# Kernel tuning notes

Measured on AMD Instinct MI355X. Metric: run time of the kernel, lower is better.

## Reference

```python
import jax, jax.numpy as jnp
import numpy as np
from jax import lax

SCORE_THRESH = 0.05
NMS_THRESH = 0.5
DETECTIONS_PER_IMG = 100
MIN_SIZE = 0.01
AREA_THRESH = 0.0
BOX_W = (10.0, 10.0, 5.0, 5.0)
BBOX_XFORM_CLIP = float(np.log(1000.0 / 16.0))


def setup_inputs() -> dict:
    key = jax.random.key(0)
    B, N, C = 8, 4000, 91
    H, W = 800, 1333
    k1, k2, k3 = jax.random.split(key, 3)
    # scale logits so a realistic fraction of softmax scores exceed score_thresh
    class_logits = jax.random.normal(k1, (B * N, C), jnp.float32) * 2.0
    box_regression = jax.random.normal(k2, (B * N, C * 4), jnp.float32)
    u = jax.random.uniform(k3, (B, N, 4), jnp.float32)
    x1 = u[..., 0] * (W - 50)
    y1 = u[..., 1] * (H - 50)
    bw = u[..., 2] * 200.0 + 4.0
    bh = u[..., 3] * 200.0 + 4.0
    proposals = jnp.stack([x1, y1, jnp.minimum(x1 + bw, W), jnp.minimum(y1 + bh, H)], axis=-1)
    return {"class_logits": class_logits, "box_regression": box_regression,
            "proposals": proposals, "image_h": H, "image_w": W}


def _decode(rel, props):
    # torchvision BoxCoder.decode: props [P,4], rel [P, C*4] -> [P, C, 4]
    w = props[:, 2] - props[:, 0]
    h = props[:, 3] - props[:, 1]
    cx = props[:, 0] + 0.5 * w
    cy = props[:, 1] + 0.5 * h
    rel = rel.reshape(rel.shape[0], -1, 4)
    dx = rel[..., 0] / BOX_W[0]
    dy = rel[..., 1] / BOX_W[1]
    dw = jnp.minimum(rel[..., 2] / BOX_W[2], BBOX_XFORM_CLIP)
    dh = jnp.minimum(rel[..., 3] / BOX_W[3], BBOX_XFORM_CLIP)
    pcx = dx * w[:, None] + cx[:, None]
    pcy = dy * h[:, None] + cy[:, None]
    pw = jnp.exp(dw) * w[:, None]
    ph = jnp.exp(dh) * h[:, None]
    return jnp.stack([pcx - 0.5 * pw, pcy - 0.5 * ph, pcx + 0.5 * pw, pcy + 0.5 * ph], axis=-1)


def _nms_image(boxes, scores, labels_f, valid, off_unit):
    # greedy batched NMS (class-offset trick) producing first DETECTIONS_PER_IMG survivors
    NEG = -1e9
    s0 = jnp.where(valid, scores, NEG)
    ob = boxes + (labels_f * off_unit)[:, None]  # per-class coordinate offset
    areas = (ob[:, 2] - ob[:, 0]) * (ob[:, 3] - ob[:, 1])

    def step(s, _):
        i = jnp.argmax(s)
        sc = s[i]
        ok = sc > (NEG / 2)
        obi = ob[i]
        ix1 = jnp.maximum(obi[0], ob[:, 0])
        iy1 = jnp.maximum(obi[1], ob[:, 1])
        ix2 = jnp.minimum(obi[2], ob[:, 2])
        iy2 = jnp.minimum(obi[3], ob[:, 3])
        inter = jnp.maximum(ix2 - ix1, 0.0) * jnp.maximum(iy2 - iy1, 0.0)
        ai = (obi[2] - obi[0]) * (obi[3] - obi[1])
        iou = inter / jnp.maximum(ai + areas - inter, 1e-9)
        sup = (iou > NMS_THRESH) & ok
        s = jnp.where(sup, NEG, s).at[i].set(NEG)
        return s, (i, jnp.where(ok, sc, 0.0), ok)

    _, (idx, out_sc, ok) = lax.scan(step, s0, None, length=DETECTIONS_PER_IMG)
    out_boxes = boxes[idx] * ok[:, None]
    out_labels = jnp.where(ok, labels_f[idx], 0.0)
    areas_out = (out_boxes[:, 2] - out_boxes[:, 0]) * (out_boxes[:, 3] - out_boxes[:, 1])
    keep = ok & (areas_out >= AREA_THRESH)
    return out_boxes * keep[:, None], out_sc * keep, jnp.where(keep, out_labels, 0.0), keep


def reference(class_logits, box_regression, proposals, image_h, image_w):
    B, N, _ = proposals.shape
    C = class_logits.shape[-1]
    pred_boxes = _decode(box_regression, proposals.reshape(B * N, 4)).reshape(B, N, C, 4)
    pred_scores = jax.nn.softmax(class_logits, axis=-1).reshape(B, N, C)
    # clip boxes to image
    x = jnp.clip(pred_boxes[..., 0::2], 0.0, float(image_w))
    y = jnp.clip(pred_boxes[..., 1::2], 0.0, float(image_h))
    pred_boxes = jnp.stack([x[..., 0], y[..., 0], x[..., 1], y[..., 1]], axis=-1)
    # drop background class 0, flatten (proposal, class) pairs
    M = N * (C - 1)
    boxes = pred_boxes[:, :, 1:, :].reshape(B, M, 4)
    scores = pred_scores[:, :, 1:].reshape(B, M)
    labels_f = jnp.broadcast_to(jnp.arange(1, C, dtype=boxes.dtype)[None, :], (N, C - 1)).reshape(M)
    ws = boxes[..., 2] - boxes[..., 0]
    hs = boxes[..., 3] - boxes[..., 1]
    valid = (scores > SCORE_THRESH) & (ws >= MIN_SIZE) & (hs >= MIN_SIZE)
    off_unit = float(max(image_h, image_w)) + 1.0
    out_boxes, out_scores, out_labels_f, keep = jax.vmap(
        lambda b, s, v: _nms_image(b, s, labels_f, v, off_unit))(boxes, scores, valid)
    return out_boxes, out_scores, out_labels_f.astype(jnp.int32), keep
```

## Files before the change

kernel.cpp:

```cpp
#include <hip/hip_runtime.h>
#include <stdint.h>

typedef uint32_t u32;
typedef unsigned long long u64;

#define NB 8
#define NPER 4000
#define NC 91
#define NCLS 90
#define NDET 100
#define CHUNKS 64
#define RPB 63
#define LBIN 16
#define CCAP 63
#define BINCAP 512
#define SURVCAP 9216
#define NSFIX (NCLS * NDET)
#define FKCAP 1024
#define VPT 36

__device__ __forceinline__ float4 decode_clip(float4 rel, float w, float h,
                                              float cx, float cy, float W, float H) {
  const float XCLIP = 4.135166556742356f;
  float dx = rel.x / 10.0f;
  float dy = rel.y / 10.0f;
  float dw = fminf(rel.z / 5.0f, XCLIP);
  float dh = fminf(rel.w / 5.0f, XCLIP);
  float qcx = dx * w + cx;
  float qcy = dy * h + cy;
  float qw = expf(dw) * w;
  float qh = expf(dh) * h;
  float x1 = qcx - 0.5f * qw, y1 = qcy - 0.5f * qh;
  float x2 = qcx + 0.5f * qw, y2 = qcy + 0.5f * qh;
  x1 = fminf(fmaxf(x1, 0.0f), W);
  x2 = fminf(fmaxf(x2, 0.0f), W);
  y1 = fminf(fmaxf(y1, 0.0f), H);
  y2 = fminf(fmaxf(y2, 0.0f), H);
  return make_float4(x1, y1, x2, y2);
}

__device__ __forceinline__ float rdlane(float v, int sl) {
  return __int_as_float(__builtin_amdgcn_readlane(__float_as_int(v), sl));
}

__global__ __launch_bounds__(1024) void k_score(const float* __restrict__ logits,
    const float* __restrict__ boxreg, const float* __restrict__ props,
    const int* __restrict__ dh, const int* __restrict__ dw,
    u32* cnt_g, u64* bins_key, float4* bins_box) {
  __shared__ u64 s_key[NCLS][LBIN];
  __shared__ float4 s_box[NCLS][LBIN];
  __shared__ u32 s_cnt[NCLS];
  int tid = threadIdx.x;
  int b = blockIdx.x / CHUNKS;
  int chunk = blockIdx.x % CHUNKS;
  int wave = tid >> 6, lane = tid & 63;
  if (tid < NCLS) s_cnt[tid] = 0u;
  __syncthreads();

  float H = (float)dh[0], W = (float)dw[0];
  const float4* props4 = (const float4*)props;
  const float4* breg4 = (const float4*)boxreg;
  size_t chbase = ((size_t)(b * CHUNKS + chunk)) * NCLS;

  for (int rloc = wave; rloc < RPB; rloc += 16) {
    int rl = chunk * RPB + rloc;
    if (rl >= NPER) break;
    int r = b * NPER + rl;
    const float* lrow = logits + (size_t)r * NC;
    float xA = lrow[lane];
    float xB = (lane < NC - 64) ? lrow[64 + lane] : -3.0e38f;
    float mx = fmaxf(xA, xB);
    for (int o = 32; o; o >>= 1) mx = fmaxf(mx, __shfl_xor(mx, o));
    float eA = expf(xA - mx);
    float eB = (lane < NC - 64) ? expf(xB - mx) : 0.0f;
    float sm = eA + eB;
    for (int o = 32; o; o >>= 1) sm += __shfl_xor(sm, o);
    float sA = eA / sm;
    float sB = eB / sm;
    bool eA_ok = (lane >= 1) && (sA > 0.05f);
    bool eB_ok = (lane < NC - 64) && (sB > 0.05f);
    if (eA_ok || eB_ok) {
      float4 p = props4[r];
      float w = p.z - p.x, h = p.w - p.y;
      float cx = p.x + 0.5f * w, cy = p.y + 0.5f * h;
      if (eA_ok) {
        float4 raw = decode_clip(breg4[(size_t)r * NC + lane], w, h, cx, cy, W, H);
        if (((raw.z - raw.x) >= 0.01f) && ((raw.w - raw.y) >= 0.01f)) {
          int ci = lane - 1;
          u32 orig = (u32)(rl * NCLS + ci);
          u64 key = ((u64)__float_as_uint(sA) << 22) | (u64)(0x3FFFFFu - orig);
          u32 lp = atomicAdd(&s_cnt[ci], 1u);
          if (lp < LBIN) { s_key[ci][lp] = key; s_box[ci][lp] = raw; }
          else if (lp < CCAP) {
            size_t o = (chbase + ci) * CCAP + lp;
            bins_key[o] = key; bins_box[o] = raw;
          }
        }
      }
      if (eB_ok) {
        float4 raw = decode_clip(breg4[(size_t)r * NC + 64 + lane], w, h, cx, cy, W, H);
        if (((raw.z - raw.x) >= 0.01f) && ((raw.w - raw.y) >= 0.01f)) {
          int ci = 63 + lane;
          u32 orig = (u32)(rl * NCLS + ci);
          u64 key = ((u64)__float_as_uint(sB) << 22) | (u64)(0x3FFFFFu - orig);
          u32 lp = atomicAdd(&s_cnt[ci], 1u);
          if (lp < LBIN) { s_key[ci][lp] = key; s_box[ci][lp] = raw; }
          else if (lp < CCAP) {
            size_t o = (chbase + ci) * CCAP + lp;
            bins_key[o] = key; bins_box[o] = raw;
          }
        }
      }
    }
  }
  __syncthreads();
  if (tid < NCLS) cnt_g[chbase + tid] = s_cnt[tid];
  for (int idx = tid; idx < NCLS * LBIN; idx += 1024) {
    int ci = idx / LBIN, j = idx % LBIN;
    if ((u32)j < s_cnt[ci]) {
      size_t o = (chbase + ci) * CCAP + (u32)j;
      bins_key[o] = s_key[ci][j];
      bins_box[o] = s_box[ci][j];
    }
  }
}

__global__ __launch_bounds__(256) void k_nms_class(const u32* __restrict__ cnt_g,
    const u64* __restrict__ bins_key, const float4* __restrict__ bins_box,
    u64* skey, float4* sbox, const int* __restrict__ dh, const int* __restrict__ dw) {
  __shared__ u64 k[BINCAP];
  __shared__ float4 boxu[BINCAP];
  __shared__ u64 ks[BINCAP];
  __shared__ float4 boxs[BINCAP];
  __shared__ float4 s_sb[NDET];
  __shared__ float s_sa[NDET];
  __shared__ u64 s_sk[NDET];
  __shared__ u32 s_sid[NDET];
  __shared__ u32 s_n;

  int b = blockIdx.x / NCLS;
  int ci = blockIdx.x % NCLS;
  int tid = threadIdx.x;
  u64* outk = skey + (size_t)b * SURVCAP + (size_t)ci * NDET;
  float4* outb = sbox + (size_t)b * SURVCAP + (size_t)ci * NDET;

  if (tid < 64) {
    u32 cntc = cnt_g[((size_t)(b * CHUNKS + tid)) * NCLS + ci];
    if (cntc > CCAP) cntc = CCAP;
    u32 inc = cntc;
    for (int o = 1; o < 64; o <<= 1) {
      u32 v = __shfl_up(inc, o);
      if (tid >= o) inc += v;
    }
    u32 off = inc - cntc;
    if (tid == 63) s_n = inc;
    size_t src = (((size_t)(b * CHUNKS + tid)) * NCLS + ci) * CCAP;
    for (u32 i = 0; i < cntc; ++i) {
      u32 d = off + i;
      if (d < BINCAP) { k[d] = bins_key[src + i]; boxu[d] = bins_box[src + i]; }
    }
  }
  __syncthreads();
  int n = (int)s_n;
  if (n > BINCAP) n = BINCAP;
  if (n <= 0) {
    for (int i = tid; i < NDET; i += 256) outk[i] = 0ull;
    return;
  }
  for (int i = tid; i < n; i += 256) {
    u64 ki = k[i];
    u32 rank = 0;
    int j = 0;
    for (; j + 4 <= n; j += 4) {
      rank += (k[j] > ki) ? 1u : 0u;
      rank += (k[j + 1] > ki) ? 1u : 0u;
      rank += (k[j + 2] > ki) ? 1u : 0u;
      rank += (k[j + 3] > ki) ? 1u : 0u;
    }
    for (; j < n; ++j) rank += (k[j] > ki) ? 1u : 0u;
    ks[rank] = ki;
    boxs[rank] = boxu[i];
  }
  __syncthreads();
  if (tid >= 64) return;

  float H = (float)dh[0], W = (float)dw[0];
  float loff = (fmaxf(H, W) + 1.0f) * (float)(ci + 1);
  int lane = tid;
  int S = 0;
  for (int base = 0; base < n && S < NDET; base += 64) {
    int i = base + lane;
    bool have = (i < n);
    u64 mykey = 0ull;
    float4 Bb = make_float4(0.f, 0.f, 0.f, 0.f);
    float aB = 0.f;
    if (have) {
      mykey = ks[i];
      float4 raw = boxs[i];
      Bb = make_float4(raw.x + loff, raw.y + loff, raw.z + loff, raw.w + loff);
      aB = (Bb.z - Bb.x) * (Bb.w - Bb.y);
    }
    bool alive = have;
    for (int s = 0; s < S; ++s) {
      float4 A = s_sb[s];
      float aA = s_sa[s];
      float ix1 = fmaxf(A.x, Bb.x), iy1 = fmaxf(A.y, Bb.y);
      float ix2 = fminf(A.z, Bb.z), iy2 = fminf(A.w, Bb.w);
      float inter = fmaxf(ix2 - ix1, 0.0f) * fmaxf(iy2 - iy1, 0.0f);
      float iou = inter / fmaxf(aA + aB - inter, 1e-9f);
      if (alive && iou > 0.5f) alive = false;
    }
    u64 mask = __ballot(alive);
    while (mask && S < NDET) {
      int j = __builtin_ctzll(mask);
      int js = __builtin_amdgcn_readfirstlane(j);
      float Ax = rdlane(Bb.x, js), Ay = rdlane(Bb.y, js);
      float Az = rdlane(Bb.z, js), Aw = rdlane(Bb.w, js);
      float aA = rdlane(aB, js);
      if (lane == js) {
        s_sb[S] = Bb; s_sa[S] = aB; s_sk[S] = mykey; s_sid[S] = (u32)i;
      }
      float ix1 = fmaxf(Ax, Bb.x), iy1 = fmaxf(Ay, Bb.y);
      float ix2 = fminf(Az, Bb.z), iy2 = fminf(Aw, Bb.w);
      float inter = fmaxf(ix2 - ix1, 0.0f) * fmaxf(iy2 - iy1, 0.0f);
      float iou = inter / fmaxf(aA + aB - inter, 1e-9f);
      if (alive && iou > 0.5f) alive = false;
      ++S;
      mask = __ballot(alive);
    }
  }
  for (int i2 = lane; i2 < NDET; i2 += 64) {
    if (i2 < S) {
      outk[i2] = s_sk[i2];
      outb[i2] = boxs[s_sid[i2]];
    } else {
      outk[i2] = 0ull;
    }
  }
}

__global__ __launch_bounds__(256) void k_top(const u64* __restrict__ skey,
    const float4* __restrict__ sbox, float* out) {
  __shared__ u32 ssc[SURVCAP];
  __shared__ u32 s_red[4];
  __shared__ u32 s_cnt[2];
  __shared__ u64 fk[FKCAP];
  __shared__ u32 fs[FKCAP];
  __shared__ u64 okey[NDET];
  __shared__ u32 osrc[NDET];

  int b = blockIdx.x;
  int tid = threadIdx.x;
  const u64* kb = skey + (size_t)b * SURVCAP;

  u32 sc[VPT];
#pragma unroll
  for (int v = 0; v < VPT; ++v) {
    u32 j = (u32)tid + (u32)v * 256u;
    u32 s = 0u;
    if (j < NSFIX) s = (u32)(kb[j] >> 22);
    sc[v] = s;
    ssc[j] = s;
  }
  if (tid == 0) { s_cnt[0] = 0; s_cnt[1] = 0; }
  __syncthreads();

  u32 lo = 0x3D4CCCCEu, hi = 0x3F800001u;
  while (lo < hi) {
    u32 mid = lo + ((hi - lo) >> 1);
    u32 c = 0;
#pragma unroll
    for (int v = 0; v < VPT; ++v) c += (sc[v] > mid) ? 1u : 0u;
    for (int o = 32; o; o >>= 1) c += __shfl_xor(c, o);
    if ((tid & 63) == 0) s_red[tid >> 6] = c;
    __syncthreads();
    u32 totc = s_red[0] + s_red[1] + s_red[2] + s_red[3];
    __syncthreads();
    if (totc < NDET) hi = mid; else lo = mid + 1;
  }
  u32 T = lo;
  __syncthreads();

  for (u32 j = tid; j < NSFIX; j += 256) {
    if (ssc[j] > T) {
      u32 p = atomicAdd(&s_cnt[0], 1u);
      if (p < FKCAP) { fk[p] = kb[j]; fs[p] = j; }
    }
  }
  __syncthreads();
  if (tid == 0) s_cnt[1] = s_cnt[0];
  __syncthreads();
  for (u32 j = tid; j < NSFIX; j += 256) {
    if (ssc[j] == T) {
      u32 p = atomicAdd(&s_cnt[1], 1u);
      if (p < FKCAP) { fk[p] = kb[j]; fs[p] = j; }
    }
  }
  __syncthreads();
  u32 tot = s_cnt[1];
  if (tot > FKCAP) tot = FKCAP;
  if (tid >= 64) return;

  for (int i = tid; i < NDET; i += 64) okey[i] = 0ull;
  for (int i = tid; i < (int)tot; i += 64) {
    u64 ki = fk[i];
    u32 rank = 0;
    for (int j = 0; j < (int)tot; ++j) rank += (fk[j] > ki) ? 1u : 0u;
    if (rank < NDET) { okey[rank] = ki; osrc[rank] = fs[i]; }
  }
  for (int i = tid; i < NDET; i += 64) {
    u64 key = okey[i];
    float b0 = 0.f, b1 = 0.f, b2 = 0.f, b3 = 0.f, sc2 = 0.f, lb = 0.f, kp = 0.f;
    if (key) {
      float4 bx = sbox[(size_t)b * SURVCAP + osrc[i]];
      b0 = bx.x; b1 = bx.y; b2 = bx.z; b3 = bx.w;
      sc2 = __uint_as_float((u32)(key >> 22));
      u32 orig = 0x3FFFFFu - (u32)(key & 0x3FFFFFu);
      lb = (float)(orig % NCLS + 1u);
      kp = 1.0f;
    }
    float* ob = out + ((size_t)b * NDET + i) * 4;
    ob[0] = b0; ob[1] = b1; ob[2] = b2; ob[3] = b3;
    out[NB * NDET * 4 + b * NDET + i] = sc2;
    out[NB * NDET * 5 + b * NDET + i] = lb;
    out[NB * NDET * 6 + b * NDET + i] = kp;
  }
}

extern "C" void kernel_launch(void* const* d_in, const int* in_sizes, int n_in,
                              void* d_out, int out_size, void* d_ws, size_t ws_size,
                              hipStream_t stream) {
  const float* logits = (const float*)d_in[0];
  const float* boxreg = (const float*)d_in[1];
  const float* props  = (const float*)d_in[2];
  const int* dh = (const int*)d_in[3];
  const int* dw = (const int*)d_in[4];
  float* out = (float*)d_out;

  char* ws = (char*)d_ws;
  u32* cnt_g = (u32*)ws;
  char* p0 = ws + ((size_t)NB * CHUNKS * NCLS * 4 + 255 & ~(size_t)255);
  u64* bins_key = (u64*)p0;
  char* p1 = p0 + (size_t)NB * CHUNKS * NCLS * CCAP * 8;
  float4* bins_box = (float4*)p1;
  char* p2 = p1 + (size_t)NB * CHUNKS * NCLS * CCAP * 16;
  u64* skey = (u64*)p2;
  float4* sbox = (float4*)(p2 + (size_t)NB * SURVCAP * 8);
  (void)ws_size;

  k_score<<<NB * CHUNKS, 1024, 0, stream>>>(logits, boxreg, props, dh, dw,
                                            cnt_g, bins_key, bins_box);
  k_nms_class<<<NB * NCLS, 256, 0, stream>>>(cnt_g, bins_key, bins_box,
                                             skey, sbox, dh, dw);
  k_top<<<NB, 256, 0, stream>>>(skey, sbox, out);
}
```

Baseline: 174.2 us.

## Fuse per-image top-k into NMS kernel via last-block counter; interleave two rows

Merges the final per-image top-100 selection into the per-class NMS kernel: each block increments a per-image done counter, and the last finishing block for an image runs the top-k and output writes using a shared-memory union. This removes one kernel launch and its dependency gap. The score kernel now processes two rows per wave iteration to overlap the softmax reductions. NMS bin gathering is spread across 256 threads instead of 64. The fusion relies on threadfence and an atomic counter that is reset inside the score kernel, and the union raises shared memory use per NMS block.

```diff
diff --git a/kernel.cpp b/kernel.cpp
--- a/kernel.cpp
+++ b/kernel.cpp
@@ -43,10 +43,50 @@
   return __int_as_float(__builtin_amdgcn_readlane(__float_as_int(v), sl));
 }
 
+__device__ __forceinline__ void emit_row(int r, int rl, int lane, float sA, float sB,
+    float W, float H, const float4* __restrict__ props4, const float4* __restrict__ breg4,
+    u32* s_cnt, u64 (*s_key)[LBIN], float4 (*s_box)[LBIN],
+    size_t chbase, u64* __restrict__ bins_key, float4* __restrict__ bins_box) {
+  bool eA_ok = (lane >= 1) && (sA > 0.05f);
+  bool eB_ok = (lane < NC - 64) && (sB > 0.05f);
+  if (!(eA_ok || eB_ok)) return;
+  float4 p = props4[r];
+  float w = p.z - p.x, h = p.w - p.y;
+  float cx = p.x + 0.5f * w, cy = p.y + 0.5f * h;
+  if (eA_ok) {
+    float4 raw = decode_clip(breg4[(size_t)r * NC + lane], w, h, cx, cy, W, H);
+    if (((raw.z - raw.x) >= 0.01f) && ((raw.w - raw.y) >= 0.01f)) {
+      int ci = lane - 1;
+      u32 orig = (u32)(rl * NCLS + ci);
+      u64 key = ((u64)__float_as_uint(sA) << 22) | (u64)(0x3FFFFFu - orig);
+      u32 lp = atomicAdd(&s_cnt[ci], 1u);
+      if (lp < LBIN) { s_key[ci][lp] = key; s_box[ci][lp] = raw; }
+      else if (lp < CCAP) {
+        size_t o = (chbase + ci) * CCAP + lp;
+        bins_key[o] = key; bins_box[o] = raw;
+      }
+    }
+  }
+  if (eB_ok) {
+    float4 raw = decode_clip(breg4[(size_t)r * NC + 64 + lane], w, h, cx, cy, W, H);
+    if (((raw.z - raw.x) >= 0.01f) && ((raw.w - raw.y) >= 0.01f)) {
+      int ci = 63 + lane;
+      u32 orig = (u32)(rl * NCLS + ci);
+      u64 key = ((u64)__float_as_uint(sB) << 22) | (u64)(0x3FFFFFu - orig);
+      u32 lp = atomicAdd(&s_cnt[ci], 1u);
+      if (lp < LBIN) { s_key[ci][lp] = key; s_box[ci][lp] = raw; }
+      else if (lp < CCAP) {
+        size_t o = (chbase + ci) * CCAP + lp;
+        bins_key[o] = key; bins_box[o] = raw;
+      }
+    }
+  }
+}
+
 __global__ __launch_bounds__(1024) void k_score(const float* __restrict__ logits,
     const float* __restrict__ boxreg, const float* __restrict__ props,
     const int* __restrict__ dh, const int* __restrict__ dw,
-    u32* cnt_g, u64* bins_key, float4* bins_box) {
+    u32* cnt_g, u64* bins_key, float4* bins_box, u32* done_cnt) {
   __shared__ u64 s_key[NCLS][LBIN];
   __shared__ float4 s_box[NCLS][LBIN];
   __shared__ u32 s_cnt[NCLS];
@@ -55,6 +95,7 @@
   int chunk = blockIdx.x % CHUNKS;
   int wave = tid >> 6, lane = tid & 63;
   if (tid < NCLS) s_cnt[tid] = 0u;
+  if (chunk == 0 && tid == 0) done_cnt[b] = 0u;
   __syncthreads();
 
   float H = (float)dh[0], W = (float)dw[0];
@@ -62,56 +103,40 @@
   const float4* breg4 = (const float4*)boxreg;
   size_t chbase = ((size_t)(b * CHUNKS + chunk)) * NCLS;
 
-  for (int rloc = wave; rloc < RPB; rloc += 16) {
-    int rl = chunk * RPB + rloc;
-    if (rl >= NPER) break;
-    int r = b * NPER + rl;
-    const float* lrow = logits + (size_t)r * NC;
-    float xA = lrow[lane];
-    float xB = (lane < NC - 64) ? lrow[64 + lane] : -3.0e38f;
-    float mx = fmaxf(xA, xB);
-    for (int o = 32; o; o >>= 1) mx = fmaxf(mx, __shfl_xor(mx, o));
-    float eA = expf(xA - mx);
-    float eB = (lane < NC - 64) ? expf(xB - mx) : 0.0f;
-    float sm = eA + eB;
-    for (int o = 32; o; o >>= 1) sm += __shfl_xor(sm, o);
-    float sA = eA / sm;
-    float sB = eB / sm;
-    bool eA_ok = (lane >= 1) && (sA > 0.05f);
-    bool eB_ok = (lane < NC - 64) && (sB > 0.05f);
-    if (eA_ok || eB_ok) {
-      float4 p = props4[r];
-      float w = p.z - p.x, h = p.w - p.y;
-      float cx = p.x + 0.5f * w, cy = p.y + 0.5f * h;
-      if (eA_ok) {
-        float4 raw = decode_clip(breg4[(size_t)r * NC + lane], w, h, cx, cy, W, H);
-        if (((raw.z - raw.x) >= 0.01f) && ((raw.w - raw.y) >= 0.01f)) {
-          int ci = lane - 1;
-          u32 orig = (u32)(rl * NCLS + ci);
-          u64 key = ((u64)__float_as_uint(sA) << 22) | (u64)(0x3FFFFFu - orig);
-          u32 lp = atomicAdd(&s_cnt[ci], 1u);
-          if (lp < LBIN) { s_key[ci][lp] = key; s_box[ci][lp] = raw; }
-          else if (lp < CCAP) {
-            size_t o = (chbase + ci) * CCAP + lp;
-            bins_key[o] = key; bins_box[o] = raw;
-          }
-        }
-      }
-      if (eB_ok) {
-        float4 raw = decode_clip(breg4[(size_t)r * NC + 64 + lane], w, h, cx, cy, W, H);
-        if (((raw.z - raw.x) >= 0.01f) && ((raw.w - raw.y) >= 0.01f)) {
-          int ci = 63 + lane;
-          u32 orig = (u32)(rl * NCLS + ci);
-          u64 key = ((u64)__float_as_uint(sB) << 22) | (u64)(0x3FFFFFu - orig);
-          u32 lp = atomicAdd(&s_cnt[ci], 1u);
-          if (lp < LBIN) { s_key[ci][lp] = key; s_box[ci][lp] = raw; }
-          else if (lp < CCAP) {
-            size_t o = (chbase + ci) * CCAP + lp;
-            bins_key[o] = key; bins_box[o] = raw;
-          }
-        }
-      }
-    }
+  for (int rloc = wave; rloc < RPB; rloc += 32) {
+    int rloc1 = rloc + 16;
+    int rl0 = chunk * RPB + rloc;
+    int rl1 = chunk * RPB + rloc1;
+    bool v0 = (rl0 < NPER);
+    bool v1 = (rloc1 < RPB) && (rl1 < NPER);
+    int r0 = b * NPER + (v0 ? rl0 : 0);
+    int r1 = b * NPER + (v1 ? rl1 : 0);
+    const float* l0 = logits + (size_t)r0 * NC;
+    const float* l1 = logits + (size_t)r1 * NC;
+    float xA0 = l0[lane];
+    float xA1 = l1[lane];
+    float xB0 = (lane < NC - 64) ? l0[64 + lane] : -3.0e38f;
+    float xB1 = (lane < NC - 64) ? l1[64 + lane] : -3.0e38f;
+    float mx0 = fmaxf(xA0, xB0);
+    float mx1 = fmaxf(xA1, xB1);
+    for (int o = 32; o; o >>= 1) {
+      mx0 = fmaxf(mx0, __shfl_xor(mx0, o));
+      mx1 = fmaxf(mx1, __shfl_xor(mx1, o));
+    }
+    float eA0 = expf(xA0 - mx0);
+    float eA1 = expf(xA1 - mx1);
+    float eB0 = (lane < NC - 64) ? expf(xB0 - mx0) : 0.0f;
+    float eB1 = (lane < NC - 64) ? expf(xB1 - mx1) : 0.0f;
+    float sm0 = eA0 + eB0;
+    float sm1 = eA1 + eB1;
+    for (int o = 32; o; o >>= 1) {
+      sm0 += __shfl_xor(sm0, o);
+      sm1 += __shfl_xor(sm1, o);
+    }
+    if (v0) emit_row(r0, rl0, lane, eA0 / sm0, eB0 / sm0, W, H, props4, breg4,
+                     s_cnt, s_key, s_box, chbase, bins_key, bins_box);
+    if (v1) emit_row(r1, rl1, lane, eA1 / sm1, eB1 / sm1, W, H, props4, breg4,
+                     s_cnt, s_key, s_box, chbase, bins_key, bins_box);
   }
   __syncthreads();
   if (tid < NCLS) cnt_g[chbase + tid] = s_cnt[tid];
@@ -125,18 +150,37 @@
   }
 }
 
-__global__ __launch_bounds__(256) void k_nms_class(const u32* __restrict__ cnt_g,
+struct NmsSh {
+  u64 k[BINCAP];
+  u64 ks[BINCAP];
+  float4 boxu[BINCAP];
+  float4 boxs[BINCAP];
+  float4 s_sb[NDET];
+  u64 s_sk[NDET];
+  float s_sa[NDET];
+  u32 s_sid[NDET];
+  u32 off[64];
+  u32 cnt[64];
+  u32 s_n;
+};
+struct TopSh {
+  u32 ssc[SURVCAP];
+  u64 fk[FKCAP];
+  u32 fs[FKCAP];
+  u64 okey[NDET];
+  u32 osrc[NDET];
+  u32 s_red[4];
+  u32 s_cnt[2];
+};
+#define SMEM_BYTES (sizeof(TopSh) > sizeof(NmsSh) ? sizeof(TopSh) : sizeof(NmsSh))
+
+__global__ __launch_bounds__(256) void k_nms(const u32* __restrict__ cnt_g,
     const u64* __restrict__ bins_key, const float4* __restrict__ bins_box,
-    u64* skey, float4* sbox, const int* __restrict__ dh, const int* __restrict__ dw) {
-  __shared__ u64 k[BINCAP];
-  __shared__ float4 boxu[BINCAP];
-  __shared__ u64 ks[BINCAP];
-  __shared__ float4 boxs[BINCAP];
-  __shared__ float4 s_sb[NDET];
-  __shared__ float s_sa[NDET];
-  __shared__ u64 s_sk[NDET];
-  __shared__ u32 s_sid[NDET];
-  __shared__ u32 s_n;
+    u64* skey, float4* sbox, u32* done_cnt,
+    const int* __restrict__ dh, const int* __restrict__ dw, float* out) {
+  __shared__ __align__(16) char smem[SMEM_BYTES];
+  __shared__ u32 s_last;
+  NmsSh& N = *reinterpret_cast<NmsSh*>(smem);
 
   int b = blockIdx.x / NCLS;
   int ci = blockIdx.x % NCLS;
@@ -145,114 +189,112 @@
   float4* outb = sbox + (size_t)b * SURVCAP + (size_t)ci * NDET;
 
   if (tid < 64) {
-    u32 cntc = cnt_g[((size_t)(b * CHUNKS + tid)) * NCLS + ci];
-    if (cntc > CCAP) cntc = CCAP;
-    u32 inc = cntc;
+    u32 c = cnt_g[((size_t)(b * CHUNKS + tid)) * NCLS + ci];
+    if (c > CCAP) c = CCAP;
+    N.cnt[tid] = c;
+    u32 inc = c;
     for (int o = 1; o < 64; o <<= 1) {
       u32 v = __shfl_up(inc, o);
       if (tid >= o) inc += v;
     }
-    u32 off = inc - cntc;
-    if (tid == 63) s_n = inc;
-    size_t src = (((size_t)(b * CHUNKS + tid)) * NCLS + ci) * CCAP;
-    for (u32 i = 0; i < cntc; ++i) {
-      u32 d = off + i;
-      if (d < BINCAP) { k[d] = bins_key[src + i]; boxu[d] = bins_box[src + i]; }
-    }
-  }
-  __syncthreads();
-  int n = (int)s_n;
-  if (n > BINCAP) n = BINCAP;
-  if (n <= 0) {
+    N.off[tid] = inc - c;
+    if (tid == 63) N.s_n = (inc > BINCAP) ? BINCAP : inc;
+  }
+  __syncthreads();
+  int n = (int)N.s_n;
+  if (n > 0) {
+    {
+      int chunk = tid & 63, start = tid >> 6;
+      u32 cc = N.cnt[chunk], of = N.off[chunk];
+      size_t src = (((size_t)(b * CHUNKS + chunk)) * NCLS + ci) * CCAP;
+      for (u32 i = (u32)start; i < cc; i += 4) {
+        u32 d = of + i;
+        if (d < (u32)BINCAP) { N.k[d] = bins_key[src + i]; N.boxu[d] = bins_box[src + i]; }
+      }
+    }
+    __syncthreads();
+    for (int i = tid; i < n; i += 256) {
+      u64 ki = N.k[i];
+      u32 rank = 0;
+      int j = 0;
+      for (; j + 4 <= n; j += 4) {
+        rank += (N.k[j] > ki) ? 1u : 0u;
+        rank += (N.k[j + 1] > ki) ? 1u : 0u;
+        rank += (N.k[j + 2] > ki) ? 1u : 0u;
+        rank += (N.k[j + 3] > ki) ? 1u : 0u;
+      }
+      for (; j < n; ++j) rank += (N.k[j] > ki) ? 1u : 0u;
+      N.ks[rank] = ki;
+      N.boxs[rank] = N.boxu[i];
+    }
+    __syncthreads();
+    if (tid < 64) {
+      float H = (float)dh[0], W = (float)dw[0];
+      float loff = (fmaxf(H, W) + 1.0f) * (float)(ci + 1);
+      int lane = tid;
+      int S = 0;
+      for (int base = 0; base < n && S < NDET; base += 64) {
+        int i = base + lane;
+        bool have = (i < n);
+        u64 mykey = 0ull;
+        float4 Bb = make_float4(0.f, 0.f, 0.f, 0.f);
+        float aB = 0.f;
+        if (have) {
+          mykey = N.ks[i];
+          float4 raw = N.boxs[i];
+          Bb = make_float4(raw.x + loff, raw.y + loff, raw.z + loff, raw.w + loff);
+          aB = (Bb.z - Bb.x) * (Bb.w - Bb.y);
+        }
+        bool alive = have;
+        for (int s = 0; s < S; ++s) {
+          float4 A = N.s_sb[s];
+          float aA = N.s_sa[s];
+          float ix1 = fmaxf(A.x, Bb.x), iy1 = fmaxf(A.y, Bb.y);
+          float ix2 = fminf(A.z, Bb.z), iy2 = fminf(A.w, Bb.w);
+          float inter = fmaxf(ix2 - ix1, 0.0f) * fmaxf(iy2 - iy1, 0.0f);
+          float iou = inter / fmaxf(aA + aB - inter, 1e-9f);
+          if (alive && iou > 0.5f) alive = false;
+        }
+        u64 mask = __ballot(alive);
+        while (mask && S < NDET) {
+          int j = __builtin_ctzll(mask);
+          int js = __builtin_amdgcn_readfirstlane(j);
+          float Ax = rdlane(Bb.x, js), Ay = rdlane(Bb.y, js);
+          float Az = rdlane(Bb.z, js), Aw = rdlane(Bb.w, js);
+          float aA = rdlane(aB, js);
+          if (lane == js) {
+            N.s_sb[S] = Bb; N.s_sa[S] = aB; N.s_sk[S] = mykey; N.s_sid[S] = (u32)i;
+          }
+          float ix1 = fmaxf(Ax, Bb.x), iy1 = fmaxf(Ay, Bb.y);
+          float ix2 = fminf(Az, Bb.z), iy2 = fminf(Aw, Bb.w);
+          float inter = fmaxf(ix2 - ix1, 0.0f) * fmaxf(iy2 - iy1, 0.0f);
+          float iou = inter / fmaxf(aA + aB - inter, 1e-9f);
+          if (alive && iou > 0.5f) alive = false;
+          ++S;
+          mask = __ballot(alive);
+        }
+      }
+      for (int i2 = lane; i2 < NDET; i2 += 64) {
+        if (i2 < S) {
+          outk[i2] = N.s_sk[i2];
+          outb[i2] = N.boxs[N.s_sid[i2]];
+        } else {
+          outk[i2] = 0ull;
+        }
+      }
+    }
+  } else {
     for (int i = tid; i < NDET; i += 256) outk[i] = 0ull;
-    return;
-  }
-  for (int i = tid; i < n; i += 256) {
-    u64 ki = k[i];
-    u32 rank = 0;
-    int j = 0;
-    for (; j + 4 <= n; j += 4) {
-      rank += (k[j] > ki) ? 1u : 0u;
-      rank += (k[j + 1] > ki) ? 1u : 0u;
-      rank += (k[j + 2] > ki) ? 1u : 0u;
-      rank += (k[j + 3] > ki) ? 1u : 0u;
-    }
-    for (; j < n; ++j) rank += (k[j] > ki) ? 1u : 0u;
-    ks[rank] = ki;
-    boxs[rank] = boxu[i];
-  }
-  __syncthreads();
-  if (tid >= 64) return;
-
-  float H = (float)dh[0], W = (float)dw[0];
-  float loff = (fmaxf(H, W) + 1.0f) * (float)(ci + 1);
-  int lane = tid;
-  int S = 0;
-  for (int base = 0; base < n && S < NDET; base += 64) {
-    int i = base + lane;
-    bool have = (i < n);
-    u64 mykey = 0ull;
-    float4 Bb = make_float4(0.f, 0.f, 0.f, 0.f);
-    float aB = 0.f;
-    if (have) {
-      mykey = ks[i];
-      float4 raw = boxs[i];
-      Bb = make_float4(raw.x + loff, raw.y + loff, raw.z + loff, raw.w + loff);
-      aB = (Bb.z - Bb.x) * (Bb.w - Bb.y);
-    }
-    bool alive = have;
-    for (int s = 0; s < S; ++s) {
-      float4 A = s_sb[s];
-      float aA = s_sa[s];
-      float ix1 = fmaxf(A.x, Bb.x), iy1 = fmaxf(A.y, Bb.y);
-      float ix2 = fminf(A.z, Bb.z), iy2 = fminf(A.w, Bb.w);
-      float inter = fmaxf(ix2 - ix1, 0.0f) * fmaxf(iy2 - iy1, 0.0f);
-      float iou = inter / fmaxf(aA + aB - inter, 1e-9f);
-      if (alive && iou > 0.5f) alive = false;
-    }
-    u64 mask = __ballot(alive);
-    while (mask && S < NDET) {
-      int j = __builtin_ctzll(mask);
-      int js = __builtin_amdgcn_readfirstlane(j);
-      float Ax = rdlane(Bb.x, js), Ay = rdlane(Bb.y, js);
-      float Az = rdlane(Bb.z, js), Aw = rdlane(Bb.w, js);
-      float aA = rdlane(aB, js);
-      if (lane == js) {
-        s_sb[S] = Bb; s_sa[S] = aB; s_sk[S] = mykey; s_sid[S] = (u32)i;
-      }
-      float ix1 = fmaxf(Ax, Bb.x), iy1 = fmaxf(Ay, Bb.y);
-      float ix2 = fminf(Az, Bb.z), iy2 = fminf(Aw, Bb.w);
-      float inter = fmaxf(ix2 - ix1, 0.0f) * fmaxf(iy2 - iy1, 0.0f);
-      float iou = inter / fmaxf(aA + aB - inter, 1e-9f);
-      if (alive && iou > 0.5f) alive = false;
-      ++S;
-      mask = __ballot(alive);
-    }
-  }
-  for (int i2 = lane; i2 < NDET; i2 += 64) {
-    if (i2 < S) {
-      outk[i2] = s_sk[i2];
-      outb[i2] = boxs[s_sid[i2]];
-    } else {
-      outk[i2] = 0ull;
-    }
-  }
-}
-
-__global__ __launch_bounds__(256) void k_top(const u64* __restrict__ skey,
-    const float4* __restrict__ sbox, float* out) {
-  __shared__ u32 ssc[SURVCAP];
-  __shared__ u32 s_red[4];
-  __shared__ u32 s_cnt[2];
-  __shared__ u64 fk[FKCAP];
-  __shared__ u32 fs[FKCAP];
-  __shared__ u64 okey[NDET];
-  __shared__ u32 osrc[NDET];
-
-  int b = blockIdx.x;
-  int tid = threadIdx.x;
+  }
+  __threadfence();
+  __syncthreads();
+  if (tid == 0) s_last = atomicAdd(done_cnt + b, 1u);
+  __syncthreads();
+  if (s_last != (u32)(NCLS - 1)) return;
+  __threadfence();
+
+  TopSh& T2 = *reinterpret_cast<TopSh*>(smem);
   const u64* kb = skey + (size_t)b * SURVCAP;
-
   u32 sc[VPT];
 #pragma unroll
   for (int v = 0; v < VPT; ++v) {
@@ -260,9 +302,9 @@
     u32 s = 0u;
     if (j < NSFIX) s = (u32)(kb[j] >> 22);
     sc[v] = s;
-    ssc[j] = s;
-  }
-  if (tid == 0) { s_cnt[0] = 0; s_cnt[1] = 0; }
+    T2.ssc[j] = s;
+  }
+  if (tid == 0) { T2.s_cnt[0] = 0; T2.s_cnt[1] = 0; }
   __syncthreads();
 
   u32 lo = 0x3D4CCCCEu, hi = 0x3F800001u;
@@ -272,9 +314,9 @@
 #pragma unroll
     for (int v = 0; v < VPT; ++v) c += (sc[v] > mid) ? 1u : 0u;
     for (int o = 32; o; o >>= 1) c += __shfl_xor(c, o);
-    if ((tid & 63) == 0) s_red[tid >> 6] = c;
+    if ((tid & 63) == 0) T2.s_red[tid >> 6] = c;
     __syncthreads();
-    u32 totc = s_red[0] + s_red[1] + s_red[2] + s_red[3];
+    u32 totc = T2.s_red[0] + T2.s_red[1] + T2.s_red[2] + T2.s_red[3];
     __syncthreads();
     if (totc < NDET) hi = mid; else lo = mid + 1;
   }
@@ -282,37 +324,37 @@
   __syncthreads();
 
   for (u32 j = tid; j < NSFIX; j += 256) {
-    if (ssc[j] > T) {
-      u32 p = atomicAdd(&s_cnt[0], 1u);
-      if (p < FKCAP) { fk[p] = kb[j]; fs[p] = j; }
-    }
-  }
-  __syncthreads();
-  if (tid == 0) s_cnt[1] = s_cnt[0];
+    if (T2.ssc[j] > T) {
+      u32 p = atomicAdd(&T2.s_cnt[0], 1u);
+      if (p < FKCAP) { T2.fk[p] = kb[j]; T2.fs[p] = j; }
+    }
+  }
+  __syncthreads();
+  if (tid == 0) T2.s_cnt[1] = T2.s_cnt[0];
   __syncthreads();
   for (u32 j = tid; j < NSFIX; j += 256) {
-    if (ssc[j] == T) {
-      u32 p = atomicAdd(&s_cnt[1], 1u);
-      if (p < FKCAP) { fk[p] = kb[j]; fs[p] = j; }
-    }
-  }
-  __syncthreads();
-  u32 tot = s_cnt[1];
+    if (T2.ssc[j] == T) {
+      u32 p = atomicAdd(&T2.s_cnt[1], 1u);
+      if (p < FKCAP) { T2.fk[p] = kb[j]; T2.fs[p] = j; }
+    }
+  }
+  __syncthreads();
+  u32 tot = T2.s_cnt[1];
   if (tot > FKCAP) tot = FKCAP;
   if (tid >= 64) return;
 
-  for (int i = tid; i < NDET; i += 64) okey[i] = 0ull;
+  for (int i = tid; i < NDET; i += 64) T2.okey[i] = 0ull;
   for (int i = tid; i < (int)tot; i += 64) {
-    u64 ki = fk[i];
+    u64 ki = T2.fk[i];
     u32 rank = 0;
-    for (int j = 0; j < (int)tot; ++j) rank += (fk[j] > ki) ? 1u : 0u;
-    if (rank < NDET) { okey[rank] = ki; osrc[rank] = fs[i]; }
+    for (int j = 0; j < (int)tot; ++j) rank += (T2.fk[j] > ki) ? 1u : 0u;
+    if (rank < NDET) { T2.okey[rank] = ki; T2.osrc[rank] = T2.fs[i]; }
   }
   for (int i = tid; i < NDET; i += 64) {
-    u64 key = okey[i];
+    u64 key = T2.okey[i];
     float b0 = 0.f, b1 = 0.f, b2 = 0.f, b3 = 0.f, sc2 = 0.f, lb = 0.f, kp = 0.f;
     if (key) {
-      float4 bx = sbox[(size_t)b * SURVCAP + osrc[i]];
+      float4 bx = sbox[(size_t)b * SURVCAP + T2.osrc[i]];
       b0 = bx.x; b1 = bx.y; b2 = bx.z; b3 = bx.w;
       sc2 = __uint_as_float((u32)(key >> 22));
       u32 orig = 0x3FFFFFu - (u32)(key & 0x3FFFFFu);
@@ -339,7 +381,8 @@
 
   char* ws = (char*)d_ws;
   u32* cnt_g = (u32*)ws;
-  char* p0 = ws + ((size_t)NB * CHUNKS * NCLS * 4 + 255 & ~(size_t)255);
+  u32* done_cnt = (u32*)(ws + ((size_t)NB * CHUNKS * NCLS * 4));
+  char* p0 = ws + (((size_t)NB * CHUNKS * NCLS * 4 + 64 + 255) & ~(size_t)255);
   u64* bins_key = (u64*)p0;
   char* p1 = p0 + (size_t)NB * CHUNKS * NCLS * CCAP * 8;
   float4* bins_box = (float4*)p1;
@@ -349,8 +392,7 @@
   (void)ws_size;
 
   k_score<<<NB * CHUNKS, 1024, 0, stream>>>(logits, boxreg, props, dh, dw,
-                                            cnt_g, bins_key, bins_box);
-  k_nms_class<<<NB * NCLS, 256, 0, stream>>>(cnt_g, bins_key, bins_box,
-                                             skey, sbox, dh, dw);
-  k_top<<<NB, 256, 0, stream>>>(skey, sbox, out);
-}
+                                            cnt_g, bins_key, bins_box, done_cnt);
+  k_nms<<<NB * NCLS, 256, 0, stream>>>(cnt_g, bins_key, bins_box,
+                                       skey, sbox, done_cnt, dh, dw, out);
+}
```

Result: slower. 195.3 us (+12.2%).
